# Kernel tuning notes

Measured on AMD Instinct MI355X. Metric: run time of the kernel, lower is better.

## Reference

```python
import jax, jax.numpy as jnp
import numpy as np

B, S, H, W, C = 1, 14, 56, 56, 192
WS = 7            # cubic window
SH = 3            # shift
HEADS = 6
HD = C // HEADS
N = WS ** 3       # 343 tokens per window
NW = (S // WS) * (H // WS) * (W // WS)  # 128 windows
SCALE = HD ** -0.5
HID = 4 * C
TBL = (2 * WS - 1) ** 3  # 2197


def _rel_index():
    # faithful to torch: meshgrid with indexing='xy' and the (3*ws-1)/(2*ws-1) strides
    c = np.stack(np.meshgrid(np.arange(WS), np.arange(WS), np.arange(WS), indexing='xy'))
    f = c.reshape(3, -1)                      # (3, N)
    r = (f[:, :, None] - f[:, None, :]).transpose(1, 2, 0)  # (N, N, 3)
    r = r + (WS - 1)
    r[..., 0] *= 3 * WS - 1
    r[..., 1] *= 2 * WS - 1
    return jnp.asarray(r.sum(-1), dtype=jnp.int32)  # (N, N)

REL_IDX = _rel_index()


def _ln(x, g, b):
    m = x.mean(-1, keepdims=True)
    v = ((x - m) ** 2).mean(-1, keepdims=True)
    return (x - m) * jax.lax.rsqrt(v + 1e-5) * g + b


def _partition(x):  # (B,S,H,W,C) -> (B*nW, N, C)
    x = x.reshape(B, S // WS, WS, H // WS, WS, W // WS, WS, C)
    x = x.transpose(0, 1, 3, 5, 2, 4, 6, 7)
    return x.reshape(-1, N, C)


def _reverse(w):  # (B*nW, N, C) -> (B,S,H,W,C)
    x = w.reshape(B, S // WS, H // WS, W // WS, WS, WS, WS, C)
    x = x.transpose(0, 1, 4, 2, 5, 3, 6, 7)
    return x.reshape(B, S, H, W, C)


def setup_inputs() -> dict:
    key = jax.random.key(0)
    ks = jax.random.split(key, 16)
    L = S * H * W
    p = lambda k, shp, s=0.02: (jax.random.normal(k, shp, dtype=jnp.float32) * s)
    return {
        'x': jax.random.normal(ks[0], (B, L, C), dtype=jnp.float32),
        'mask_matrix': jax.random.normal(ks[1], (NW, N, N), dtype=jnp.float32),
        'skip': jax.random.normal(ks[2], (B, L, C), dtype=jnp.float32),
        'x_up': jax.random.normal(ks[3], (B, L, C), dtype=jnp.float32),
        'norm1_g': jnp.ones((C,), jnp.float32),
        'norm1_b': jnp.zeros((C,), jnp.float32),
        'kv_w': p(ks[4], (C, 2 * C)),
        'kv_b': jnp.zeros((2 * C,), jnp.float32),
        'rel_bias_table': p(ks[5], (TBL, HEADS)),
        'proj_w': p(ks[6], (C, C)),
        'proj_b': jnp.zeros((C,), jnp.float32),
        'norm2_g': jnp.ones((C,), jnp.float32),
        'norm2_b': jnp.zeros((C,), jnp.float32),
        'fc1_w': p(ks[7], (C, HID)),
        'fc1_b': jnp.zeros((HID,), jnp.float32),
        'fc2_w': p(ks[8], (HID, C)),
        'fc2_b': jnp.zeros((C,), jnp.float32),
    }


def reference(x, mask_matrix, skip, x_up, norm1_g, norm1_b, kv_w, kv_b,
              rel_bias_table, proj_w, proj_b, norm2_g, norm2_b,
              fc1_w, fc1_b, fc2_w, fc2_b):
    shortcut = x
    sk = _ln(skip, norm1_g, norm1_b).reshape(B, S, H, W, C)
    xu = _ln(x_up, norm1_g, norm1_b).reshape(B, S, H, W, C)
    # cyclic shift (shift_size > 0, dims divisible by window -> no padding)
    sk = jnp.roll(sk, (-SH, -SH, -SH), axis=(1, 2, 3))
    xu = jnp.roll(xu, (-SH, -SH, -SH), axis=(1, 2, 3))
    sk_w = _partition(sk)   # (Bw, N, C)
    xu_w = _partition(xu)
    Bw = sk_w.shape[0]
    kv = (sk_w @ kv_w + kv_b).reshape(Bw, N, 2, HEADS, HD)
    k = kv[:, :, 0].transpose(0, 2, 1, 3)   # (Bw, h, N, d)
    v = kv[:, :, 1].transpose(0, 2, 1, 3)
    q = xu_w.reshape(Bw, N, HEADS, HD).transpose(0, 2, 1, 3) * SCALE
    attn = jnp.einsum('bhnd,bhmd->bhnm', q, k)
    bias = rel_bias_table[REL_IDX].transpose(2, 0, 1)  # (h, N, N)
    attn = attn + bias[None]
    attn = attn.reshape(B, NW, HEADS, N, N) + mask_matrix[None, :, None]
    attn = jax.nn.softmax(attn.reshape(Bw, HEADS, N, N), axis=-1)
    out = jnp.einsum('bhnm,bhmd->bhnd', attn, v)
    out = out.transpose(0, 2, 1, 3).reshape(Bw, N, C)
    out = out @ proj_w + proj_b
    xr = _reverse(out)
    xr = jnp.roll(xr, (SH, SH, SH), axis=(1, 2, 3)).reshape(B, S * H * W, C)
    x = shortcut + xr
    h = _ln(x, norm2_g, norm2_b)
    h = jax.nn.gelu(h @ fc1_w + fc1_b, approximate=False) @ fc2_w + fc2_b
    return x + h
```

## Files before the change

kernel.cpp:

```cpp
#include <hip/hip_runtime.h>
#include <cstddef>

typedef unsigned short u16;
typedef unsigned int   u32;
typedef __bf16 bf16_t;
typedef bf16_t bf16x8 __attribute__((ext_vector_type(8)));
typedef short  s16x4  __attribute__((ext_vector_type(4)));
typedef float  f32x4  __attribute__((ext_vector_type(4)));
typedef u16    u16x4  __attribute__((ext_vector_type(4)));

#define NPAD 352
#define VTS  352
#define LOG2E 1.4426950408889634f
#define RESCALE_THR 11.5f

__device__ __forceinline__ u16 f2b(float f) {
  return __builtin_bit_cast(u16, (__bf16)f);
}
__device__ __forceinline__ float b2f(u16 h) {
  return __uint_as_float(((u32)h) << 16);
}
__device__ __forceinline__ float fexp2(float x) {
#if __has_builtin(__builtin_amdgcn_exp2f)
  return __builtin_amdgcn_exp2f(x);
#else
  float r; asm("v_exp_f32 %0, %1" : "=v"(r) : "v"(x)); return r;
#endif
}
__device__ __forceinline__ f32x4 mfma16(bf16x8 a, bf16x8 b, f32x4 c) {
  return __builtin_amdgcn_mfma_f32_16x16x32_bf16(a, b, c, 0, 0, 0);
}
__device__ __forceinline__ f32x4 mfma16x16(s16x4 a, s16x4 b, f32x4 c) {
#if __has_builtin(__builtin_amdgcn_mfma_f32_16x16x16bf16_1k)
  return __builtin_amdgcn_mfma_f32_16x16x16bf16_1k(a, b, c, 0, 0, 0);
#else
  f32x4 d;
  asm volatile("v_mfma_f32_16x16x16_bf16 %0, %1, %2, %3"
               : "=&v"(d) : "v"(a), "v"(b), "v"(c));
  return d;
#endif
}
__device__ __forceinline__ void gl_lds16(const void* g, void* l) {
  __builtin_amdgcn_global_load_lds((const __attribute__((address_space(1))) void*)g,
                                   (__attribute__((address_space(3))) void*)l, 16, 0, 0);
}

__device__ __forceinline__ int win_to_global(int w, int n) {
  int ws = w >> 6, wh = (w >> 3) & 7, ww = w & 7;
  int ts = (n * 1338) >> 16;
  int rem = n - ts * 49;
  int th = (rem * 9363) >> 16;
  int tw = rem - th * 7;
  int gs = ws * 7 + ts + 3; if (gs >= 14) gs -= 14;
  int gh = wh * 7 + th + 3; if (gh >= 56) gh -= 56;
  int gw = ww * 7 + tw + 3; if (gw >= 56) gw -= 56;
  return (gs * 56 + gh) * 56 + gw;
}

#define MC_END 15488
#define LN_END (MC_END + 10976)
#define WC_END (LN_END + 1824)
#define PRE_GRID (WC_END + 726)

__global__ __launch_bounds__(256) void k_pre(
    const float* __restrict__ mask, u16* __restrict__ mb,
    const float* __restrict__ skip, const float* __restrict__ xup,
    const float* __restrict__ g1, const float* __restrict__ b1,
    u16* __restrict__ skw, u16* __restrict__ qb,
    const float* __restrict__ kv_w, const float* __restrict__ proj_w,
    const float* __restrict__ fc1_w, const float* __restrict__ fc2_w,
    u16* kvT, u16* projT, u16* fc1T, u16* fc2T,
    const float* __restrict__ tbl, u16* __restrict__ bf) {
  int bid = blockIdx.x, tid = threadIdx.x;
  if (bid < MC_END) {
    int t = bid * 256 + tid;
    int w = t / (352 * 88);
    int r = t - w * (352 * 88);
    int n = r / 88;
    int q = r - n * 88;
    u16x4 v = {0, 0, 0, 0};
    if (n < 343) {
      const float* src = mask + ((size_t)w * 343 + n) * 343 + q * 4;
      #pragma unroll
      for (int j = 0; j < 4; ++j) if (q * 4 + j < 343) v[j] = f2b(src[j] * LOG2E);
    }
    *(u16x4*)&mb[((size_t)w * 352 + n) * 352 + q * 4] = v;
  } else if (bid < LN_END) {
    int wid = tid >> 6, lane = tid & 63;
    int m = (bid - MC_END) * 4 + wid;
    u32 w = ((u32)m * 48914u) >> 24;
    int n = m - (int)w * 343;
    int g = win_to_global((int)w, n);
    float xs[3], xu[3];
    float s1 = 0.f, s2 = 0.f, t1 = 0.f, t2 = 0.f;
    #pragma unroll
    for (int i = 0; i < 3; ++i) {
      int c = lane + i * 64;
      xs[i] = skip[(size_t)g * 192 + c];
      xu[i] = xup[(size_t)g * 192 + c];
      s1 += xs[i]; s2 += xs[i] * xs[i];
      t1 += xu[i]; t2 += xu[i] * xu[i];
    }
    #pragma unroll
    for (int off = 1; off < 64; off <<= 1) {
      s1 += __shfl_xor(s1, off); s2 += __shfl_xor(s2, off);
      t1 += __shfl_xor(t1, off); t2 += __shfl_xor(t2, off);
    }
    const float inv = 1.f / 192.f;
    float ms = s1 * inv, vs = s2 * inv - ms * ms;
    float mu = t1 * inv, vu = t2 * inv - mu * mu;
    float rs = rsqrtf(vs + 1e-5f), ru = rsqrtf(vu + 1e-5f);
    #pragma unroll
    for (int i = 0; i < 3; ++i) {
      int c = lane + i * 64;
      float gg = g1[c], bb = b1[c];
      skw[(size_t)m * 192 + c] = f2b((xs[i] - ms) * rs * gg + bb);
      float qv = ((xu[i] - mu) * ru * gg + bb) * 0.25503513f;
      int h = c >> 5, d = c & 31;
      qb[(size_t)(((int)w * 6 + h) * NPAD + n) * 32 + d] = f2b(qv);
    }
  } else if (bid < WC_END) {
    int t = (bid - LN_END) * 256 + tid;
    if (t < 384 * 192) { int nn = t / 192, kk = t - nn * 192; kvT[t] = f2b(kv_w[kk * 384 + nn]); return; }
    t -= 384 * 192;
    if (t < 256 * 192) { int nn = t / 192, kk = t - nn * 192; projT[t] = (nn < 192) ? f2b(proj_w[kk * 192 + nn]) : (u16)0; return; }
    t -= 256 * 192;
    if (t < 768 * 192) { int nn = t / 192, kk = t - nn * 192; fc1T[t] = f2b(fc1_w[kk * 768 + nn]); return; }
    t -= 768 * 192;
    if (t < 256 * 768) { int nn = t / 768, kk = t - nn * 768; fc2T[t] = (nn < 192) ? f2b(fc2_w[kk * 192 + nn]) : (u16)0; return; }
  } else {
    int t = (bid - WC_END) * 256 + tid;
    int h = t / (352 * 88);
    int r = t - h * (352 * 88);
    int n = r / 88;
    int q = r - n * 88;
    u16x4 v = {0, 0, 0, 0};
    if (n < 343 && h < 6) {
      int tsn = (n * 1338) >> 16, remn = n - tsn * 49, thn = (remn * 9363) >> 16, twn = remn - thn * 7;
      #pragma unroll
      for (int j = 0; j < 4; ++j) {
        int m = q * 4 + j;
        if (m < 343) {
          int tsm = (m * 1338) >> 16, remm = m - tsm * 49, thm = (remm * 9363) >> 16, twm = remm - thm * 7;
          int idx = (thn - thm) * 20 + (tsn - tsm) * 13 + (twn - twm) + 204;
          v[j] = f2b(tbl[idx * 6 + h] * LOG2E);
        }
      }
    }
    if (h < 6) *(u16x4*)&bf[((size_t)h * 352 + n) * 352 + q * 4] = v;
  }
}

__global__ __launch_bounds__(256) void k_ln2(const float* __restrict__ xr,
    const float* __restrict__ g2, const float* __restrict__ b2, u16* __restrict__ o) {
  int wid = threadIdx.x >> 6, lane = threadIdx.x & 63;
  int m = blockIdx.x * 4 + wid;
  float v[3]; float s1 = 0.f, s2 = 0.f;
  #pragma unroll
  for (int i = 0; i < 3; ++i) {
    int c = lane + i * 64;
    v[i] = xr[(size_t)m * 192 + c];
    s1 += v[i]; s2 += v[i] * v[i];
  }
  #pragma unroll
  for (int off = 1; off < 64; off <<= 1) { s1 += __shfl_xor(s1, off); s2 += __shfl_xor(s2, off); }
  const float inv = 1.f / 192.f;
  float ms = s1 * inv, vs = s2 * inv - ms * ms;
  float rs = rsqrtf(vs + 1e-5f);
  #pragma unroll
  for (int i = 0; i < 3; ++i) {
    int c = lane + i * 64;
    o[(size_t)m * 192 + c] = f2b((v[i] - ms) * rs * g2[c] + b2[c]);
  }
}

template<int EPI>
__global__ __launch_bounds__(256) void k_gemm(
    const u16* __restrict__ A, const u16* __restrict__ Bm, int K, int nbn,
    const float* __restrict__ bias,
    u16* __restrict__ outa, u16* __restrict__ outb,
    const float* __restrict__ xin, float* __restrict__ xres,
    float* __restrict__ outf) {
  __shared__ __align__(16) u16 As[128 * 32];
  __shared__ __align__(16) u16 Bs[128 * 32];
  int bid = blockIdx.x;
  int xcd = bid & 7, j = bid >> 3;
  int bn = j % nbn, bmL = j / nbn;
  int bm = xcd * 43 + bmL;
  if (bm >= 343) return;
  int tid = threadIdx.x;
  int wid = tid >> 6, lane = tid & 63, lr = lane & 15, lg = lane >> 4;
  int wr = wid >> 1, wc = wid & 1;
  f32x4 acc[4][4] = {};
  const u16* Abase = A + (size_t)bm * 128 * K;
  const u16* Bbase = Bm + (size_t)bn * 128 * K;
  int nk = K >> 5;
  for (int kt = 0; kt < nk; ++kt) {
    int ci0 = tid, ci1 = tid + 256;
    int r0 = ci0 >> 2, c0 = (ci0 & 3) * 8;
    int r1 = ci1 >> 2, c1 = (ci1 & 3) * 8;
    gl_lds16(Abase + (size_t)r0 * K + kt * 32 + c0, &As[ci0 * 8]);
    gl_lds16(Abase + (size_t)r1 * K + kt * 32 + c1, &As[ci1 * 8]);
    gl_lds16(Bbase + (size_t)r0 * K + kt * 32 + c0, &Bs[ci0 * 8]);
    gl_lds16(Bbase + (size_t)r1 * K + kt * 32 + c1, &Bs[ci1 * 8]);
    __syncthreads();
    bf16x8 af[4], bfr[4];
    #pragma unroll
    for (int mi = 0; mi < 4; ++mi) af[mi] = *(const bf16x8*)&As[(wr * 64 + mi * 16 + lr) * 32 + lg * 8];
    #pragma unroll
    for (int ni = 0; ni < 4; ++ni) bfr[ni] = *(const bf16x8*)&Bs[(wc * 64 + ni * 16 + lr) * 32 + lg * 8];
    #pragma unroll
    for (int mi = 0; mi < 4; ++mi)
      #pragma unroll
      for (int ni = 0; ni < 4; ++ni)
        acc[mi][ni] = mfma16(af[mi], bfr[ni], acc[mi][ni]);
    __syncthreads();
  }
  #pragma unroll
  for (int mi = 0; mi < 4; ++mi) {
    #pragma unroll
    for (int r = 0; r < 4; ++r) {
      int grow = bm * 128 + wr * 64 + mi * 16 + lg * 4 + r;
      if (EPI == 0) {
        u32 w = ((u32)grow * 48914u) >> 24; int n = grow - (int)w * 343;
        #pragma unroll
        for (int ni = 0; ni < 4; ++ni) {
          int gcol = bn * 128 + wc * 64 + ni * 16 + lr;
          float v = acc[mi][ni][r] + bias[gcol];
          if (gcol < 192) {
            int hh = gcol >> 5, d = gcol & 31;
            int dswz = ((((d >> 3) ^ ((n >> 1) & 3)) << 3) | (d & 7));
            outa[(size_t)(((int)w * 6 + hh) * NPAD + n) * 32 + dswz] = f2b(v);
          } else {
            int c2 = gcol - 192; int hh = c2 >> 5, d = c2 & 31;
            int nswz = ((((n >> 3) ^ ((d >> 1) & 3)) << 3) | (n & 7));
            outb[(size_t)(((int)w * 6 + hh) * 32 + d) * VTS + nswz] = f2b(v);
          }
        }
      } else if (EPI == 1) {
        #pragma unroll
        for (int ni = 0; ni < 4; ++ni) {
          int gcol = bn * 128 + wc * 64 + ni * 16 + lr;
          if (gcol < 192) {
            float v = acc[mi][ni][r] + bias[gcol] + xin[(size_t)grow * 192 + gcol];
            xres[(size_t)grow * 192 + gcol] = v;
          }
        }
      } else if (EPI == 2) {
        #pragma unroll
        for (int ni = 0; ni < 4; ++ni) {
          int gcol = bn * 128 + wc * 64 + ni * 16 + lr;
          float v = acc[mi][ni][r] + bias[gcol];
          v = 0.5f * v * (1.f + erff(v * 0.7071067811865476f));
          outa[(size_t)grow * 768 + gcol] = f2b(v);
        }
      } else {
        #pragma unroll
        for (int ni = 0; ni < 4; ++ni) {
          int gcol = bn * 128 + wc * 64 + ni * 16 + lr;
          if (gcol < 192)
            outf[(size_t)grow * 192 + gcol] = acc[mi][ni][r] + bias[gcol] + xin[(size_t)grow * 192 + gcol];
        }
      }
    }
  }
}

template<int CT0, int LEN, bool TAIL, bool FIRST>
__device__ __forceinline__ void attn_chunk(const u16* __restrict__ Ks, const u16* __restrict__ Vs,
    bf16x8 qa, int lr, int lg, int swz,
    const u16* __restrict__ brow, const u16* __restrict__ mrow,
    f32x4& o0, f32x4& o1, float& mrun, float& sum) {
  u16x4 bb[LEN], mm[LEN];
  #pragma unroll
  for (int j = 0; j < LEN; ++j) {
    bb[j] = *(const u16x4*)&brow[(CT0 + j) * 16];
    mm[j] = *(const u16x4*)&mrow[(CT0 + j) * 16];
  }
  f32x4 s[LEN];
  const f32x4 z = {0.f, 0.f, 0.f, 0.f};
  __builtin_amdgcn_s_setprio(1);
  #pragma unroll
  for (int j = 0; j < LEN; ++j) {
    bf16x8 kf = *(const bf16x8*)&Ks[((CT0 + j) * 16 + lr) * 32 + (lg ^ swz) * 8];
    s[j] = mfma16(kf, qa, z);
  }
  __builtin_amdgcn_s_setprio(0);
  #pragma unroll
  for (int j = 0; j < LEN; ++j)
    #pragma unroll
    for (int r = 0; r < 4; ++r) s[j][r] += b2f(bb[j][r]) + b2f(mm[j][r]);
  if (TAIL) {
    int m0 = 336 + lg * 4;
    #pragma unroll
    for (int r = 0; r < 4; ++r) if (m0 + r >= 343) s[LEN - 1][r] = -1e30f;
  }
  float mloc = -1e30f;
  #pragma unroll
  for (int j = 0; j < LEN; ++j)
    mloc = fmaxf(mloc, fmaxf(fmaxf(s[j][0], s[j][1]), fmaxf(s[j][2], s[j][3])));
  if (FIRST) {
    mloc = fmaxf(mloc, __shfl_xor(mloc, 16));
    mloc = fmaxf(mloc, __shfl_xor(mloc, 32));
    mrun = mloc;
  } else if (!__all(mloc <= mrun + RESCALE_THR)) {
    mloc = fmaxf(mloc, __shfl_xor(mloc, 16));
    mloc = fmaxf(mloc, __shfl_xor(mloc, 32));
    float mnew = fmaxf(mrun, mloc);
    float sc = fexp2(mrun - mnew);
    #pragma unroll
    for (int r = 0; r < 4; ++r) {
      float scr = __shfl(sc, lg * 4 + r);
      o0[r] *= scr; o1[r] *= scr;
    }
    sum *= sc;
    mrun = mnew;
  }
  #pragma unroll
  for (int j = 0; j < LEN; ++j)
    #pragma unroll
    for (int r = 0; r < 4; ++r) { float p = fexp2(s[j][r] - mrun); s[j][r] = p; sum += p; }
  __builtin_amdgcn_s_setprio(1);
  #pragma unroll
  for (int j = 0; j < LEN; ++j) {
    s16x4 pa;
    #pragma unroll
    for (int r = 0; r < 4; ++r) pa[r] = (short)f2b(s[j][r]);
    int c16 = 2 * (CT0 + j) + (lg >> 1);
    int vo = ((c16 ^ swz) * 8) + (lg & 1) * 4;
    s16x4 v0 = *(const s16x4*)&Vs[lr * 352 + vo];
    s16x4 v1 = *(const s16x4*)&Vs[(16 + lr) * 352 + vo];
    o0 = mfma16x16(pa, v0, o0);
    o1 = mfma16x16(pa, v1, o1);
  }
  __builtin_amdgcn_s_setprio(0);
}

__global__ __launch_bounds__(256, 2) void k_attn(const u16* __restrict__ qb, const u16* __restrict__ kb,
    const u16* __restrict__ vtb, const u16* __restrict__ bfull, const u16* __restrict__ maskbf,
    u16* __restrict__ att) {
  __shared__ __align__(16) u16 Ks[352 * 32];
  __shared__ __align__(16) u16 Vs[32 * 352];
  __shared__ __align__(16) u16 Ot[4][16][40];
  int bid = blockIdx.x;
  int xcd = bid & 7, i = bid >> 3;
  int wl = i / 6, h = i - wl * 6;
  int w = xcd * 16 + wl;
  int tid = threadIdx.x, wid = tid >> 6, lane = tid & 63, lr = lane & 15, lg = lane >> 4;
  const u16* Q  = qb  + (size_t)(w * 6 + h) * NPAD * 32;
  const u16* Kg = kb  + (size_t)(w * 6 + h) * NPAD * 32;
  const u16* Vg = vtb + (size_t)(w * 6 + h) * 32 * VTS;
  const u16* Bp = bfull + (size_t)h * 352 * 352;
  const u16* Mp = maskbf + (size_t)w * 352 * 352;
  #pragma unroll
  for (int it = 0; it < 11; ++it) {
    int idx = it * 256 + tid;
    if (idx < 1408) gl_lds16(Kg + idx * 8, &Ks[idx * 8]);
    else            gl_lds16(Vg + (idx - 1408) * 8, &Vs[(idx - 1408) * 8]);
  }
  __syncthreads();
  int swz = (lr >> 1) & 3;
  for (int rt = wid; rt < 22; rt += 4) {
    int n = rt * 16 + lr;
    bf16x8 qa = *(const bf16x8*)&Q[(size_t)n * 32 + lg * 8];
    const u16* brow = Bp + (size_t)n * 352 + lg * 4;
    const u16* mrow = Mp + (size_t)n * 352 + lg * 4;
    f32x4 o0 = {0.f, 0.f, 0.f, 0.f}, o1 = {0.f, 0.f, 0.f, 0.f};
    float mrun = -1e30f, sum = 0.f;
    attn_chunk<0,  6, false, true >(Ks, Vs, qa, lr, lg, swz, brow, mrow, o0, o1, mrun, sum);
    attn_chunk<6,  6, false, false>(Ks, Vs, qa, lr, lg, swz, brow, mrow, o0, o1, mrun, sum);
    attn_chunk<12, 6, false, false>(Ks, Vs, qa, lr, lg, swz, brow, mrow, o0, o1, mrun, sum);
    attn_chunk<18, 4, true,  false>(Ks, Vs, qa, lr, lg, swz, brow, mrow, o0, o1, mrun, sum);
    sum += __shfl_xor(sum, 16);
    sum += __shfl_xor(sum, 32);
    float rs = 1.f / sum;
    #pragma unroll
    for (int r = 0; r < 4; ++r) {
      float rsr = __shfl(rs, lg * 4 + r);
      Ot[wid][lg * 4 + r][lr] = f2b(o0[r] * rsr);
      Ot[wid][lg * 4 + r][16 + lr] = f2b(o1[r] * rsr);
    }
    if (n < 343) {
      int g = win_to_global(w, n);
      bf16x8 ov = *(const bf16x8*)&Ot[wid][lr][lg * 8];
      *(bf16x8*)&att[(size_t)g * 192 + h * 32 + lg * 8] = ov;
    }
  }
}

static const size_t OFF_W    = 0;
static const size_t OFF_XRES = (size_t)1 << 20;
static const size_t OFF_MASK = OFF_XRES;
static const size_t OFF_LN2  = OFF_XRES + ((size_t)34 << 20);
static const size_t OFF_SKW  = OFF_LN2  + ((size_t)17 << 20);
static const size_t OFF_Q    = OFF_SKW  + ((size_t)17 << 20);
static const size_t OFF_K    = OFF_Q    + ((size_t)17 << 20);
static const size_t OFF_VT   = OFF_K    + ((size_t)17 << 20);
static const size_t OFF_ATT  = OFF_VT   + ((size_t)17 << 20);
static const size_t OFF_BIAS = OFF_ATT  + ((size_t)17 << 20);
static const size_t OFF_FC1  = OFF_SKW;

extern "C" void kernel_launch(void* const* d_in, const int* in_sizes, int n_in,
                              void* d_out, int out_size, void* d_ws, size_t ws_size,
                              hipStream_t stream) {
  const float* x      = (const float*)d_in[0];
  const float* mask   = (const float*)d_in[1];
  const float* skip   = (const float*)d_in[2];
  const float* xup    = (const float*)d_in[3];
  const float* n1g    = (const float*)d_in[4];
  const float* n1b    = (const float*)d_in[5];
  const float* kv_w   = (const float*)d_in[6];
  const float* kv_b   = (const float*)d_in[7];
  const float* tbl    = (const float*)d_in[8];
  const float* proj_w = (const float*)d_in[9];
  const float* proj_b = (const float*)d_in[10];
  const float* n2g    = (const float*)d_in[11];
  const float* n2b    = (const float*)d_in[12];
  const float* fc1_w  = (const float*)d_in[13];
  const float* fc1_b  = (const float*)d_in[14];
  const float* fc2_w  = (const float*)d_in[15];
  const float* fc2_b  = (const float*)d_in[16];
  char* ws = (char*)d_ws;
  u16* kvT   = (u16*)(ws + OFF_W);
  u16* projT = kvT + 384 * 192;
  u16* fc1T  = projT + 256 * 192;
  u16* fc2T  = fc1T + 768 * 192;
  float* xres = (float*)(ws + OFF_XRES);
  u16* maskbf = (u16*)(ws + OFF_MASK);
  u16* ln2o  = (u16*)(ws + OFF_LN2);
  u16* skw   = (u16*)(ws + OFF_SKW);
  u16* qb    = (u16*)(ws + OFF_Q);
  u16* kb    = (u16*)(ws + OFF_K);
  u16* vt    = (u16*)(ws + OFF_VT);
  u16* att   = (u16*)(ws + OFF_ATT);
  u16* bfull = (u16*)(ws + OFF_BIAS);
  u16* fc1o  = (u16*)(ws + OFF_FC1);
  float* outp = (float*)d_out;

  k_pre<<<dim3(PRE_GRID), dim3(256), 0, stream>>>(
      mask, maskbf, skip, xup, n1g, n1b, skw, qb,
      kv_w, proj_w, fc1_w, fc2_w, kvT, projT, fc1T, fc2T, tbl, bfull);
  k_gemm<0><<<dim3(8 * 43 * 3), dim3(256), 0, stream>>>(skw, kvT, 192, 3, kv_b, kb, vt, nullptr, nullptr, nullptr);
  k_attn<<<dim3(768), dim3(256), 0, stream>>>(qb, kb, vt, bfull, maskbf, att);
  k_gemm<1><<<dim3(8 * 43 * 2), dim3(256), 0, stream>>>(att, projT, 192, 2, proj_b, nullptr, nullptr, x, xres, nullptr);
  k_ln2<<<dim3(10976), dim3(256), 0, stream>>>(xres, n2g, n2b, ln2o);
  k_gemm<2><<<dim3(8 * 43 * 6), dim3(256), 0, stream>>>(ln2o, fc1T, 192, 6, fc1_b, fc1o, nullptr, nullptr, nullptr, nullptr);
  k_gemm<3><<<dim3(8 * 43 * 2), dim3(256), 0, stream>>>(fc1o, fc2T, 768, 2, fc2_b, nullptr, nullptr, xres, nullptr, outp);
}
```

Measured before the change: 304.9 us.

## Fuse proj GEMM with LayerNorm2, split attention rows, read V from global

```diff
diff --git a/kernel.cpp b/kernel.cpp
--- a/kernel.cpp
+++ b/kernel.cpp
@@ -148,29 +148,6 @@
       }
     }
     if (h < 6) *(u16x4*)&bf[((size_t)h * 352 + n) * 352 + q * 4] = v;
-  }
-}
-
-__global__ __launch_bounds__(256) void k_ln2(const float* __restrict__ xr,
-    const float* __restrict__ g2, const float* __restrict__ b2, u16* __restrict__ o) {
-  int wid = threadIdx.x >> 6, lane = threadIdx.x & 63;
-  int m = blockIdx.x * 4 + wid;
-  float v[3]; float s1 = 0.f, s2 = 0.f;
-  #pragma unroll
-  for (int i = 0; i < 3; ++i) {
-    int c = lane + i * 64;
-    v[i] = xr[(size_t)m * 192 + c];
-    s1 += v[i]; s2 += v[i] * v[i];
-  }
-  #pragma unroll
-  for (int off = 1; off < 64; off <<= 1) { s1 += __shfl_xor(s1, off); s2 += __shfl_xor(s2, off); }
-  const float inv = 1.f / 192.f;
-  float ms = s1 * inv, vs = s2 * inv - ms * ms;
-  float rs = rsqrtf(vs + 1e-5f);
-  #pragma unroll
-  for (int i = 0; i < 3; ++i) {
-    int c = lane + i * 64;
-    o[(size_t)m * 192 + c] = f2b((v[i] - ms) * rs * g2[c] + b2[c]);
   }
 }
 
@@ -233,17 +210,7 @@
             outa[(size_t)(((int)w * 6 + hh) * NPAD + n) * 32 + dswz] = f2b(v);
           } else {
             int c2 = gcol - 192; int hh = c2 >> 5, d = c2 & 31;
-            int nswz = ((((n >> 3) ^ ((d >> 1) & 3)) << 3) | (n & 7));
-            outb[(size_t)(((int)w * 6 + hh) * 32 + d) * VTS + nswz] = f2b(v);
-          }
-        }
-      } else if (EPI == 1) {
-        #pragma unroll
-        for (int ni = 0; ni < 4; ++ni) {
-          int gcol = bn * 128 + wc * 64 + ni * 16 + lr;
-          if (gcol < 192) {
-            float v = acc[mi][ni][r] + bias[gcol] + xin[(size_t)grow * 192 + gcol];
-            xres[(size_t)grow * 192 + gcol] = v;
+            outb[(size_t)(((int)w * 6 + hh) * 32 + d) * VTS + n] = f2b(v);
           }
         }
       } else if (EPI == 2) {
@@ -254,7 +221,7 @@
           v = 0.5f * v * (1.f + erff(v * 0.7071067811865476f));
           outa[(size_t)grow * 768 + gcol] = f2b(v);
         }
-      } else {
+      } else if (EPI == 3) {
         #pragma unroll
         for (int ni = 0; ni < 4; ++ni) {
           int gcol = bn * 128 + wc * 64 + ni * 16 + lr;
@@ -266,8 +233,99 @@
   }
 }
 
+__global__ __launch_bounds__(256) void k_proj(
+    const u16* __restrict__ A, const u16* __restrict__ Bm,
+    const float* __restrict__ bias, const float* __restrict__ x,
+    const float* __restrict__ g2, const float* __restrict__ b2,
+    float* __restrict__ xres, u16* __restrict__ ln2o) {
+  __shared__ __align__(16) u16 As[128 * 32];
+  __shared__ __align__(16) u16 Bs[192 * 32];
+  __shared__ float S[2][64][2][2];
+  int bid = blockIdx.x;
+  int xcd = bid & 7, bmL = bid >> 3;
+  int bm = xcd * 43 + bmL;
+  if (bm >= 343) return;
+  int tid = threadIdx.x;
+  int wid = tid >> 6, lane = tid & 63, lr = lane & 15, lg = lane >> 4;
+  int wr = wid >> 1, wc = wid & 1;
+  f32x4 acc[4][6] = {};
+  const u16* Abase = A + (size_t)bm * 128 * 192;
+  for (int kt = 0; kt < 6; ++kt) {
+    #pragma unroll
+    for (int it = 0; it < 5; ++it) {
+      int idx = it * 256 + tid;
+      if (idx < 512) {
+        int r0 = idx >> 2, c0 = (idx & 3) * 8;
+        gl_lds16(Abase + (size_t)r0 * 192 + kt * 32 + c0, &As[idx * 8]);
+      } else {
+        int i2 = idx - 512;
+        int r0 = i2 >> 2, c0 = (i2 & 3) * 8;
+        gl_lds16(Bm + (size_t)r0 * 192 + kt * 32 + c0, &Bs[i2 * 8]);
+      }
+    }
+    __syncthreads();
+    bf16x8 af[4], bfr[6];
+    #pragma unroll
+    for (int mi = 0; mi < 4; ++mi) af[mi] = *(const bf16x8*)&As[(wr * 64 + mi * 16 + lr) * 32 + lg * 8];
+    #pragma unroll
+    for (int ni = 0; ni < 6; ++ni) bfr[ni] = *(const bf16x8*)&Bs[(wc * 96 + ni * 16 + lr) * 32 + lg * 8];
+    #pragma unroll
+    for (int mi = 0; mi < 4; ++mi)
+      #pragma unroll
+      for (int ni = 0; ni < 6; ++ni)
+        acc[mi][ni] = mfma16(af[mi], bfr[ni], acc[mi][ni]);
+    __syncthreads();
+  }
+  #pragma unroll
+  for (int mi = 0; mi < 4; ++mi) {
+    #pragma unroll
+    for (int r = 0; r < 4; ++r) {
+      int grow = bm * 128 + wr * 64 + mi * 16 + lg * 4 + r;
+      float ps = 0.f, pss = 0.f;
+      #pragma unroll
+      for (int ni = 0; ni < 6; ++ni) {
+        int gcol = wc * 96 + ni * 16 + lr;
+        float v = acc[mi][ni][r] + bias[gcol] + x[(size_t)grow * 192 + gcol];
+        acc[mi][ni][r] = v;
+        ps += v; pss += v * v;
+      }
+      ps  += __shfl_xor(ps, 1);  pss += __shfl_xor(pss, 1);
+      ps  += __shfl_xor(ps, 2);  pss += __shfl_xor(pss, 2);
+      ps  += __shfl_xor(ps, 4);  pss += __shfl_xor(pss, 4);
+      ps  += __shfl_xor(ps, 8);  pss += __shfl_xor(pss, 8);
+      if (lr == 0) {
+        int rowL = mi * 16 + lg * 4 + r;
+        S[wr][rowL][wc][0] = ps;
+        S[wr][rowL][wc][1] = pss;
+      }
+    }
+  }
+  __syncthreads();
+  const float inv = 1.f / 192.f;
+  #pragma unroll
+  for (int mi = 0; mi < 4; ++mi) {
+    #pragma unroll
+    for (int r = 0; r < 4; ++r) {
+      int rowL = mi * 16 + lg * 4 + r;
+      int grow = bm * 128 + wr * 64 + rowL;
+      float sum = S[wr][rowL][0][0] + S[wr][rowL][1][0];
+      float ssq = S[wr][rowL][0][1] + S[wr][rowL][1][1];
+      float mean = sum * inv;
+      float var = ssq * inv - mean * mean;
+      float rsv = rsqrtf(var + 1e-5f);
+      #pragma unroll
+      for (int ni = 0; ni < 6; ++ni) {
+        int gcol = wc * 96 + ni * 16 + lr;
+        float v = acc[mi][ni][r];
+        xres[(size_t)grow * 192 + gcol] = v;
+        ln2o[(size_t)grow * 192 + gcol] = f2b((v - mean) * rsv * g2[gcol] + b2[gcol]);
+      }
+    }
+  }
+}
+
 template<int CT0, int LEN, bool TAIL, bool FIRST>
-__device__ __forceinline__ void attn_chunk(const u16* __restrict__ Ks, const u16* __restrict__ Vs,
+__device__ __forceinline__ void attn_chunk(const u16* __restrict__ Ks, const u16* __restrict__ Vg,
     bf16x8 qa, int lr, int lg, int swz,
     const u16* __restrict__ brow, const u16* __restrict__ mrow,
     f32x4& o0, f32x4& o1, float& mrun, float& sum) {
@@ -326,10 +384,8 @@
     s16x4 pa;
     #pragma unroll
     for (int r = 0; r < 4; ++r) pa[r] = (short)f2b(s[j][r]);
-    int c16 = 2 * (CT0 + j) + (lg >> 1);
-    int vo = ((c16 ^ swz) * 8) + (lg & 1) * 4;
-    s16x4 v0 = *(const s16x4*)&Vs[lr * 352 + vo];
-    s16x4 v1 = *(const s16x4*)&Vs[(16 + lr) * 352 + vo];
+    s16x4 v0 = *(const s16x4*)&Vg[(size_t)lr * VTS + (CT0 + j) * 16 + lg * 4];
+    s16x4 v1 = *(const s16x4*)&Vg[(size_t)(16 + lr) * VTS + (CT0 + j) * 16 + lg * 4];
     o0 = mfma16x16(pa, v0, o0);
     o1 = mfma16x16(pa, v1, o1);
   }
@@ -340,10 +396,10 @@
     const u16* __restrict__ vtb, const u16* __restrict__ bfull, const u16* __restrict__ maskbf,
     u16* __restrict__ att) {
   __shared__ __align__(16) u16 Ks[352 * 32];
-  __shared__ __align__(16) u16 Vs[32 * 352];
   __shared__ __align__(16) u16 Ot[4][16][40];
   int bid = blockIdx.x;
-  int xcd = bid & 7, i = bid >> 3;
+  int xcd = bid & 7, t = bid >> 3;
+  int half = t & 1, i = t >> 1;
   int wl = i / 6, h = i - wl * 6;
   int w = xcd * 16 + wl;
   int tid = threadIdx.x, wid = tid >> 6, lane = tid & 63, lr = lane & 15, lg = lane >> 4;
@@ -353,24 +409,24 @@
   const u16* Bp = bfull + (size_t)h * 352 * 352;
   const u16* Mp = maskbf + (size_t)w * 352 * 352;
   #pragma unroll
-  for (int it = 0; it < 11; ++it) {
+  for (int it = 0; it < 6; ++it) {
     int idx = it * 256 + tid;
     if (idx < 1408) gl_lds16(Kg + idx * 8, &Ks[idx * 8]);
-    else            gl_lds16(Vg + (idx - 1408) * 8, &Vs[(idx - 1408) * 8]);
   }
   __syncthreads();
   int swz = (lr >> 1) & 3;
-  for (int rt = wid; rt < 22; rt += 4) {
+  int rt_end = half * 11 + 11;
+  for (int rt = half * 11 + wid; rt < rt_end; rt += 4) {
     int n = rt * 16 + lr;
     bf16x8 qa = *(const bf16x8*)&Q[(size_t)n * 32 + lg * 8];
     const u16* brow = Bp + (size_t)n * 352 + lg * 4;
     const u16* mrow = Mp + (size_t)n * 352 + lg * 4;
     f32x4 o0 = {0.f, 0.f, 0.f, 0.f}, o1 = {0.f, 0.f, 0.f, 0.f};
     float mrun = -1e30f, sum = 0.f;
-    attn_chunk<0,  6, false, true >(Ks, Vs, qa, lr, lg, swz, brow, mrow, o0, o1, mrun, sum);
-    attn_chunk<6,  6, false, false>(Ks, Vs, qa, lr, lg, swz, brow, mrow, o0, o1, mrun, sum);
-    attn_chunk<12, 6, false, false>(Ks, Vs, qa, lr, lg, swz, brow, mrow, o0, o1, mrun, sum);
-    attn_chunk<18, 4, true,  false>(Ks, Vs, qa, lr, lg, swz, brow, mrow, o0, o1, mrun, sum);
+    attn_chunk<0,  6, false, true >(Ks, Vg, qa, lr, lg, swz, brow, mrow, o0, o1, mrun, sum);
+    attn_chunk<6,  6, false, false>(Ks, Vg, qa, lr, lg, swz, brow, mrow, o0, o1, mrun, sum);
+    attn_chunk<12, 6, false, false>(Ks, Vg, qa, lr, lg, swz, brow, mrow, o0, o1, mrun, sum);
+    attn_chunk<18, 4, true,  false>(Ks, Vg, qa, lr, lg, swz, brow, mrow, o0, o1, mrun, sum);
     sum += __shfl_xor(sum, 16);
     sum += __shfl_xor(sum, 32);
     float rs = 1.f / sum;
@@ -441,9 +497,8 @@
       mask, maskbf, skip, xup, n1g, n1b, skw, qb,
       kv_w, proj_w, fc1_w, fc2_w, kvT, projT, fc1T, fc2T, tbl, bfull);
   k_gemm<0><<<dim3(8 * 43 * 3), dim3(256), 0, stream>>>(skw, kvT, 192, 3, kv_b, kb, vt, nullptr, nullptr, nullptr);
-  k_attn<<<dim3(768), dim3(256), 0, stream>>>(qb, kb, vt, bfull, maskbf, att);
-  k_gemm<1><<<dim3(8 * 43 * 2), dim3(256), 0, stream>>>(att, projT, 192, 2, proj_b, nullptr, nullptr, x, xres, nullptr);
-  k_ln2<<<dim3(10976), dim3(256), 0, stream>>>(xres, n2g, n2b, ln2o);
+  k_attn<<<dim3(1536), dim3(256), 0, stream>>>(qb, kb, vt, bfull, maskbf, att);
+  k_proj<<<dim3(344), dim3(256), 0, stream>>>(att, projT, proj_b, x, n2g, n2b, xres, ln2o);
   k_gemm<2><<<dim3(8 * 43 * 6), dim3(256), 0, stream>>>(ln2o, fc1T, 192, 6, fc1_b, fc1o, nullptr, nullptr, nullptr, nullptr);
   k_gemm<3><<<dim3(8 * 43 * 2), dim3(256), 0, stream>>>(fc1o, fc2T, 768, 2, fc2_b, nullptr, nullptr, xres, nullptr, outp);
 }
```

After: 320.8 us. 5.2% more time.
